# Optimization experiments

Hardware: AMD Instinct MI355X
Metric: run time of the kernel (lower is better)

The kernel has to match this reference:

```python
import jax, jax.numpy as jnp
import numpy as np

N = 262144          # number of points
L = 16              # levels per encoder
F = 2               # features per level
HMAP = 1 << 19      # hashmap entries per hashed level
BASE = 32           # base grid resolution
GROWTH = 2.0        # per-level scale
OUT_DIM = L * F * 4 # 128

# Global geographic normalization ranges (GeoAdaptiveRange.global_range())
LAT = (-90.0, 90.0)
LON = (-180.0, 180.0)
ELEV = (-11000.0, 9000.0)
TIME = (0.0, 1.0)


def _layout():
    offs, ress, hashed = [], [], []
    off = 0
    for l in range(L):
        res = int(np.ceil(BASE * GROWTH ** l))
        n = res ** 3
        size = min(n, HMAP)
        size = (size + 7) // 8 * 8  # align to 8 like tcnn/gridencoder
        offs.append(off); ress.append(res); hashed.append(n > HMAP)
        off += size
    return (np.asarray(offs, np.int32), np.asarray(ress, np.int32),
            np.asarray(hashed, np.bool_), off)

OFFSETS, RESOLUTIONS, HASHED, TABLE_SIZE = _layout()

_CORNERS = np.asarray([[(i >> 0) & 1, (i >> 1) & 1, (i >> 2) & 1] for i in range(8)], np.int32)  # [8,3]
_P0, _P1, _P2 = np.uint32(1), np.uint32(2654435761), np.uint32(805459861)  # NGP spatial-hash primes


def _encode_level(u, res, offset, use_hash, table):
    # u: [N,3] in [0,1]; res/offset/use_hash: per-level scalars; table: [T,F]
    pos = u * (res - 1).astype(u.dtype)
    p0 = jnp.clip(jnp.floor(pos).astype(jnp.int32), 0, res - 2)
    w = pos - p0.astype(u.dtype)                       # [N,3] trilinear fracs
    pc = p0[None, :, :] + _CORNERS[:, None, :]          # [8,N,3]
    dense = pc[..., 0] + res * (pc[..., 1] + res * pc[..., 2])  # [8,N]
    pcu = pc.astype(jnp.uint32)
    h = (pcu[..., 0] * _P0) ^ (pcu[..., 1] * _P1) ^ (pcu[..., 2] * _P2)
    hidx = (h & jnp.uint32(HMAP - 1)).astype(jnp.int32)
    idx = jnp.where(use_hash, hidx, dense) + offset     # [8,N]
    feats = table[idx]                                  # [8,N,F] gather
    cw = jnp.where(_CORNERS[:, None, :] == 1, w[None], 1.0 - w[None]).prod(-1)  # [8,N]
    return (feats * cw[..., None]).sum(0)               # [N,F]


def hash_encode(x, table, size=1.0):
    # x: [N,3] in [-size, size] -> multi-level hash-grid features [N, L*F]
    u = jnp.clip((x + size) / (2.0 * size), 0.0, 1.0)
    per_level = jax.vmap(_encode_level, in_axes=(None, 0, 0, 0, None))(
        u, jnp.asarray(RESOLUTIONS), jnp.asarray(OFFSETS), jnp.asarray(HASHED), table)  # [L,N,F]
    return per_level.transpose(1, 0, 2).reshape(x.shape[0], L * F)


def _norm(v, lo, hi):
    return jnp.clip((v - lo) / (hi - lo), 0.0, 1.0)


def setup_inputs() -> dict:
    key = jax.random.key(0)
    ks = jax.random.split(key, 9)
    lat = jax.random.uniform(ks[0], (N,), minval=-80.0, maxval=80.0)
    lon = jax.random.uniform(ks[1], (N,), minval=-170.0, maxval=170.0)
    elev = jax.random.uniform(ks[2], (N,), minval=-100.0, maxval=3000.0)
    t = jax.random.uniform(ks[3], (N,), minval=0.0, maxval=1.0)
    reference_coords = jnp.stack([lat, lon, elev, t], -1).astype(jnp.float32)
    # small relative offsets around the reference points
    d = jax.random.normal(ks[4], (N, 4), jnp.float32) * jnp.asarray([0.5, 0.5, 50.0, 0.05], jnp.float32)
    coords = reference_coords + d
    def tbl(k):
        return jax.random.uniform(k, (TABLE_SIZE, F), jnp.float32, minval=-1e-4, maxval=1e-4)
    return {
        "coords": coords,
        "reference_coords": reference_coords,
        "xyz_table": tbl(ks[5]),
        "xyt_table": tbl(ks[6]),
        "yzt_table": tbl(ks[7]),
        "xzt_table": tbl(ks[8]),
    }


def reference(coords, reference_coords, xyz_table, xyt_table, yzt_table, xzt_table):
    rel = coords - reference_coords
    x = _norm(rel[..., 0], *LAT)
    y = _norm(rel[..., 1], *LON)
    z = _norm(rel[..., 2], *ELEV)
    t = _norm(rel[..., 3], *TIME)
    nc = jnp.stack([x, y, z, t], -1)                    # [N,4] in [0,1]
    spatial = hash_encode(nc[..., :3], xyz_table)       # [N, L*F]
    t_s = (nc[..., 3:] * 2.0 - 1.0) * 0.9               # time -> [-0.9, 0.9]
    xyzt = jnp.concatenate([nc[..., :3], t_s], -1)
    xyt = jnp.concatenate([xyzt[..., :2], xyzt[..., 3:]], -1)
    yzt = xyzt[..., 1:]
    xzt = jnp.concatenate([xyzt[..., :1], xyzt[..., 2:]], -1)
    f_xyt = hash_encode(xyt, xyt_table)
    f_yzt = hash_encode(yzt, yzt_table)
    f_xzt = hash_encode(xzt, xzt_table)
    return jnp.concatenate([spatial, f_xyt, f_yzt, f_xzt], -1)  # [N, 128]
```

## Files before the change

kernel.cpp:

```cpp
#include <hip/hip_runtime.h>
#include <stdint.h>

#define HMAP_MASK ((1u << 19) - 1u)

__global__ __launch_bounds__(256) void energy4d_kernel(
    const float4* __restrict__ coords,
    const float4* __restrict__ refc,
    const float2* __restrict__ t0,
    const float2* __restrict__ t1,
    const float2* __restrict__ t2,
    const float2* __restrict__ t3,
    float2* __restrict__ out, int npts)
{
    #pragma clang fp contract(off)

    int t = threadIdx.x;
    int si = t & 7;
    int pi = t >> 3;
    int point = blockIdx.x * 32 + pi;
    if (point >= npts) return;
    int sub = (blockIdx.y << 3) + si;
    int table_id = sub >> 4;
    int level = sub & 15;

    float4 c = coords[point];
    float4 r = refc[point];
    float rx = c.x - r.x, ry = c.y - r.y, rz = c.z - r.z, rt = c.w - r.w;

    const float R180   = 1.0f / 180.0f;
    const float R360   = 1.0f / 360.0f;
    const float R20000 = 1.0f / 20000.0f;
    float x = fminf(fmaxf((rx + 90.0f)    * R180,   0.0f), 1.0f);
    float y = fminf(fmaxf((ry + 180.0f)   * R360,   0.0f), 1.0f);
    float z = fminf(fmaxf((rz + 11000.0f) * R20000, 0.0f), 1.0f);
    float tt = fminf(fmaxf(rt, 0.0f), 1.0f);
    float ts = (tt * 2.0f - 1.0f) * 0.9f;

    float d0 = (table_id == 2) ? y : x;
    float d1 = (table_id <= 1) ? y : z;
    float d2 = (table_id == 0) ? z : ts;
    const float2* tab = (table_id == 0) ? t0
                      : (table_id == 1) ? t1
                      : (table_id == 2) ? t2 : t3;

    float u0 = fminf(fmaxf((d0 + 1.0f) * 0.5f, 0.0f), 1.0f);
    float u1 = fminf(fmaxf((d1 + 1.0f) * 0.5f, 0.0f), 1.0f);
    float u2 = fminf(fmaxf((d2 + 1.0f) * 0.5f, 0.0f), 1.0f);

    int res = 32 << level;
    float resm1 = (float)(res - 1);
    float pos0 = u0 * resm1;
    float pos1 = u1 * resm1;
    float pos2 = u2 * resm1;
    int p0 = min(max((int)floorf(pos0), 0), res - 2);
    int p1 = min(max((int)floorf(pos1), 0), res - 2);
    int p2 = min(max((int)floorf(pos2), 0), res - 2);
    float w0 = pos0 - (float)p0;
    float w1 = pos1 - (float)p1;
    float w2 = pos2 - (float)p2;

    int off = (level >= 2) ? (294912 + ((level - 2) << 19)) : (level << 15);
    bool use_hash = (level >= 2);
    const float2* tabo = tab + off;

    float om0 = 1.0f - w0, om1 = 1.0f - w1, om2 = 1.0f - w2;
    float a0 = 0.0f, a1 = 0.0f;
    uint32_t ures = (uint32_t)res;

    #pragma unroll
    for (int ci = 0; ci < 8; ++ci) {
        int cx = ci & 1, cy = (ci >> 1) & 1, cz = (ci >> 2) & 1;
        uint32_t px = (uint32_t)(p0 + cx);
        uint32_t py = (uint32_t)(p1 + cy);
        uint32_t pz = (uint32_t)(p2 + cz);
        uint32_t idx;
        if (use_hash) {
            idx = (px ^ (py * 2654435761u) ^ (pz * 805459861u)) & HMAP_MASK;
        } else {
            idx = px + ures * (py + ures * pz);
        }
        float2 f = tabo[idx];
        float ww = (cx ? w0 : om0) * (cy ? w1 : om1) * (cz ? w2 : om2);
        a0 += f.x * ww;
        a1 += f.y * ww;
    }

    float2 val = make_float2(a0, a1);
    unsigned long long bits;
    __builtin_memcpy(&bits, &val, 8);
    __builtin_nontemporal_store(bits,
        (unsigned long long*)(out + (size_t)point * 64 + sub));
}

extern "C" void kernel_launch(void* const* d_in, const int* in_sizes, int n_in,
                              void* d_out, int out_size, void* d_ws, size_t ws_size,
                              hipStream_t stream) {
    const float4* coords = (const float4*)d_in[0];
    const float4* refc   = (const float4*)d_in[1];
    const float2* t0 = (const float2*)d_in[2];
    const float2* t1 = (const float2*)d_in[3];
    const float2* t2 = (const float2*)d_in[4];
    const float2* t3 = (const float2*)d_in[5];
    float2* out = (float2*)d_out;
    int npts = in_sizes[0] / 4;
    int grid_x = (npts + 31) / 32;
    dim3 grid(grid_x, 8);
    energy4d_kernel<<<grid, 256, 0, stream>>>(coords, refc, t0, t1, t2, t3, out, npts);
}
```

Before: 829.6 us.

## Split encoding into precompute, per-XCD level-sliced gather, and transpose kernels

Replaces the single fused kernel with three kernels. The first precomputes normalized coordinates. The second gathers with each block dedicated to one (table, level) slice, with block IDs mapped so that each XCD handles fixed slices; this keeps each hash table level resident in one XCD's L2 instead of spreading every level across all XCDs. The third transposes the slice-major staging buffer into the point-major output through shared memory. This adds a workspace round trip of about 128 MB of extra traffic and two extra launches in exchange for better cache locality on the table gathers.

```diff
diff --git a/kernel.cpp b/kernel.cpp
--- a/kernel.cpp
+++ b/kernel.cpp
@@ -3,30 +3,18 @@
 
 #define HMAP_MASK ((1u << 19) - 1u)
 
-__global__ __launch_bounds__(256) void energy4d_kernel(
+
+__global__ __launch_bounds__(256) void u_precompute_kernel(
     const float4* __restrict__ coords,
     const float4* __restrict__ refc,
-    const float2* __restrict__ t0,
-    const float2* __restrict__ t1,
-    const float2* __restrict__ t2,
-    const float2* __restrict__ t3,
-    float2* __restrict__ out, int npts)
+    float4* __restrict__ uout, int npts)
 {
     #pragma clang fp contract(off)
-
-    int t = threadIdx.x;
-    int si = t & 7;
-    int pi = t >> 3;
-    int point = blockIdx.x * 32 + pi;
-    if (point >= npts) return;
-    int sub = (blockIdx.y << 3) + si;
-    int table_id = sub >> 4;
-    int level = sub & 15;
-
-    float4 c = coords[point];
-    float4 r = refc[point];
+    int p = blockIdx.x * 256 + threadIdx.x;
+    if (p >= npts) return;
+    float4 c = coords[p];
+    float4 r = refc[p];
     float rx = c.x - r.x, ry = c.y - r.y, rz = c.z - r.z, rt = c.w - r.w;
-
     const float R180   = 1.0f / 180.0f;
     const float R360   = 1.0f / 360.0f;
     const float R20000 = 1.0f / 20000.0f;
@@ -35,10 +23,34 @@
     float z = fminf(fmaxf((rz + 11000.0f) * R20000, 0.0f), 1.0f);
     float tt = fminf(fmaxf(rt, 0.0f), 1.0f);
     float ts = (tt * 2.0f - 1.0f) * 0.9f;
-
-    float d0 = (table_id == 2) ? y : x;
-    float d1 = (table_id <= 1) ? y : z;
-    float d2 = (table_id == 0) ? z : ts;
+    uout[p] = make_float4(x, y, z, ts);
+}
+
+__global__ __launch_bounds__(256) void gather_kernel(
+    const float4* __restrict__ u,
+    const float2* __restrict__ t0,
+    const float2* __restrict__ t1,
+    const float2* __restrict__ t2,
+    const float2* __restrict__ t3,
+    float2* __restrict__ stage, int npts, int chunks)
+{
+    #pragma clang fp contract(off)
+    int bid = blockIdx.x;
+    int xcd   = bid & 7;
+    int j     = bid >> 3;
+    int phase = j / chunks;
+    int chunk = j - phase * chunks;
+    int slice = phase * 8 + xcd;
+    int table_id = slice >> 4;
+    int level    = slice & 15;
+
+    int point = chunk * 256 + threadIdx.x;
+    if (point >= npts) return;
+
+    float4 uu = u[point];
+    float d0 = (table_id == 2) ? uu.y : uu.x;
+    float d1 = (table_id <= 1) ? uu.y : uu.z;
+    float d2 = (table_id == 0) ? uu.z : uu.w;
     const float2* tab = (table_id == 0) ? t0
                       : (table_id == 1) ? t1
                       : (table_id == 2) ? t2 : t3;
@@ -89,6 +101,123 @@
     unsigned long long bits;
     __builtin_memcpy(&bits, &val, 8);
     __builtin_nontemporal_store(bits,
+        (unsigned long long*)(stage + (size_t)slice * npts + point));
+}
+
+__global__ __launch_bounds__(256) void transpose_kernel(
+    const float2* __restrict__ stage,
+    float2* __restrict__ out, int npts)
+{
+    __shared__ float2 tile[64][65];
+    int pbase = blockIdx.x * 64;
+    int lane = threadIdx.x & 63;
+    int row4 = threadIdx.x >> 6;
+
+    #pragma unroll
+    for (int s = 0; s < 64; s += 4) {
+        int sub = s + row4;
+        int p = pbase + lane;
+        if (p < npts)
+            tile[sub][lane] = stage[(size_t)sub * npts + p];
+    }
+    __syncthreads();
+    #pragma unroll
+    for (int p4 = 0; p4 < 64; p4 += 4) {
+        int p = pbase + p4 + row4;
+        if (p < npts) {
+            float2 v = tile[lane][p4 + row4];
+            unsigned long long bits;
+            __builtin_memcpy(&bits, &v, 8);
+            __builtin_nontemporal_store(bits,
+                (unsigned long long*)(out + (size_t)p * 64 + lane));
+        }
+    }
+}
+
+__global__ __launch_bounds__(256) void energy4d_fallback(
+    const float4* __restrict__ coords,
+    const float4* __restrict__ refc,
+    const float2* __restrict__ t0,
+    const float2* __restrict__ t1,
+    const float2* __restrict__ t2,
+    const float2* __restrict__ t3,
+    float2* __restrict__ out, int npts)
+{
+    #pragma clang fp contract(off)
+    int t = threadIdx.x;
+    int si = t & 7;
+    int pi = t >> 3;
+    int point = blockIdx.x * 32 + pi;
+    if (point >= npts) return;
+    int sub = (blockIdx.y << 3) + si;
+    int table_id = sub >> 4;
+    int level = sub & 15;
+
+    float4 c = coords[point];
+    float4 r = refc[point];
+    float rx = c.x - r.x, ry = c.y - r.y, rz = c.z - r.z, rt = c.w - r.w;
+    const float R180   = 1.0f / 180.0f;
+    const float R360   = 1.0f / 360.0f;
+    const float R20000 = 1.0f / 20000.0f;
+    float x = fminf(fmaxf((rx + 90.0f)    * R180,   0.0f), 1.0f);
+    float y = fminf(fmaxf((ry + 180.0f)   * R360,   0.0f), 1.0f);
+    float z = fminf(fmaxf((rz + 11000.0f) * R20000, 0.0f), 1.0f);
+    float tt = fminf(fmaxf(rt, 0.0f), 1.0f);
+    float ts = (tt * 2.0f - 1.0f) * 0.9f;
+
+    float d0 = (table_id == 2) ? y : x;
+    float d1 = (table_id <= 1) ? y : z;
+    float d2 = (table_id == 0) ? z : ts;
+    const float2* tab = (table_id == 0) ? t0
+                      : (table_id == 1) ? t1
+                      : (table_id == 2) ? t2 : t3;
+
+    float u0 = fminf(fmaxf((d0 + 1.0f) * 0.5f, 0.0f), 1.0f);
+    float u1 = fminf(fmaxf((d1 + 1.0f) * 0.5f, 0.0f), 1.0f);
+    float u2 = fminf(fmaxf((d2 + 1.0f) * 0.5f, 0.0f), 1.0f);
+
+    int res = 32 << level;
+    float resm1 = (float)(res - 1);
+    float pos0 = u0 * resm1;
+    float pos1 = u1 * resm1;
+    float pos2 = u2 * resm1;
+    int p0 = min(max((int)floorf(pos0), 0), res - 2);
+    int p1 = min(max((int)floorf(pos1), 0), res - 2);
+    int p2 = min(max((int)floorf(pos2), 0), res - 2);
+    float w0 = pos0 - (float)p0;
+    float w1 = pos1 - (float)p1;
+    float w2 = pos2 - (float)p2;
+
+    int off = (level >= 2) ? (294912 + ((level - 2) << 19)) : (level << 15);
+    bool use_hash = (level >= 2);
+    const float2* tabo = tab + off;
+
+    float om0 = 1.0f - w0, om1 = 1.0f - w1, om2 = 1.0f - w2;
+    float a0 = 0.0f, a1 = 0.0f;
+    uint32_t ures = (uint32_t)res;
+
+    #pragma unroll
+    for (int ci = 0; ci < 8; ++ci) {
+        int cx = ci & 1, cy = (ci >> 1) & 1, cz = (ci >> 2) & 1;
+        uint32_t px = (uint32_t)(p0 + cx);
+        uint32_t py = (uint32_t)(p1 + cy);
+        uint32_t pz = (uint32_t)(p2 + cz);
+        uint32_t idx;
+        if (use_hash) {
+            idx = (px ^ (py * 2654435761u) ^ (pz * 805459861u)) & HMAP_MASK;
+        } else {
+            idx = px + ures * (py + ures * pz);
+        }
+        float2 f = tabo[idx];
+        float ww = (cx ? w0 : om0) * (cy ? w1 : om1) * (cz ? w2 : om2);
+        a0 += f.x * ww;
+        a1 += f.y * ww;
+    }
+
+    float2 val = make_float2(a0, a1);
+    unsigned long long bits;
+    __builtin_memcpy(&bits, &val, 8);
+    __builtin_nontemporal_store(bits,
         (unsigned long long*)(out + (size_t)point * 64 + sub));
 }
 
@@ -103,7 +232,24 @@
     const float2* t3 = (const float2*)d_in[5];
     float2* out = (float2*)d_out;
     int npts = in_sizes[0] / 4;
-    int grid_x = (npts + 31) / 32;
-    dim3 grid(grid_x, 8);
-    energy4d_kernel<<<grid, 256, 0, stream>>>(coords, refc, t0, t1, t2, t3, out, npts);
-}
+
+    size_t u_bytes     = (size_t)npts * 16;
+    size_t stage_bytes = (size_t)npts * 64 * 8;
+    size_t needed = u_bytes + stage_bytes;
+
+    if (d_ws != nullptr && ws_size >= needed) {
+        float4* uws   = (float4*)d_ws;
+        float2* stage = (float2*)((char*)d_ws + u_bytes);
+        int chunks = (npts + 255) / 256;
+
+        u_precompute_kernel<<<chunks, 256, 0, stream>>>(coords, refc, uws, npts);
+        gather_kernel<<<64 * chunks, 256, 0, stream>>>(
+            uws, t0, t1, t2, t3, stage, npts, chunks);
+        transpose_kernel<<<(npts + 63) / 64, 256, 0, stream>>>(stage, out, npts);
+    } else {
+        int grid_x = (npts + 31) / 32;
+        dim3 grid(grid_x, 8);
+        energy4d_fallback<<<grid, 256, 0, stream>>>(coords, refc, t0, t1, t2, t3,
+                                                    out, npts);
+    }
+}
```

Measured after the change: 738.7 us. 1.12x faster.
